# Optimization experiments

Hardware: AMD Instinct MI355X
Metric: run time of the kernel (lower is better)

## Reference

```python
import jax, jax.numpy as jnp
import numpy as np

H = 4        # num_heads
KNN = 10     # k_knn neighbors gathered by distance
KS = 4       # k_select top-k neighbors kept by attention score
EPS = 1e-5
BIG = 1e9


def _ln(x, g, b):
    m = x.mean(-1, keepdims=True)
    v = ((x - m) ** 2).mean(-1, keepdims=True)
    return (x - m) * jax.lax.rsqrt(v + EPS) * g + b


def _sparse_dyn_voxel_attn(x, coords, mask, w_qkv, b_qkv, w_proj, b_proj):
    # x: [B,N,C], coords: [B,N,3], mask: [B,N] bool
    B, N, C = x.shape
    dh = C // H
    qkv = x @ w_qkv + b_qkv                       # [B,N,3C]
    q, k, v = jnp.split(qkv, 3, axis=-1)
    q = q.reshape(B, N, H, dh).transpose(0, 2, 1, 3)   # [B,H,N,dh]
    k = k.reshape(B, N, H, dh).transpose(0, 2, 1, 3)
    v = v.reshape(B, N, H, dh).transpose(0, 2, 1, 3)

    # KNN over voxel coordinates; empty voxels pushed to far distance
    d2 = jnp.sum((coords[:, :, None, :] - coords[:, None, :, :]) ** 2, axis=-1)  # [B,N,N]
    d2 = jnp.where(mask[:, None, :], d2, BIG)
    _, nbr = jax.lax.top_k(-d2, KNN)              # [B,N,KNN] nearest-neighbor indices

    # gather neighbor keys/values: [B,H,N,KNN,dh]
    kn = jax.vmap(lambda a, i: a[:, i, :])(k, nbr)
    vn = jax.vmap(lambda a, i: a[:, i, :])(v, nbr)
    nmask = jax.vmap(lambda m, i: m[i])(mask, nbr)  # [B,N,KNN]

    scale = float(1.0 / np.sqrt(dh))
    scores = jnp.einsum('bhnd,bhnkd->bhnk', q, kn) * scale  # [B,H,N,KNN]
    scores = scores + jnp.where(nmask, 0.0, -BIG)[:, None, :, :]

    # dynamic selection: keep top k_select neighbors by score, softmax over them
    sv, si = jax.lax.top_k(scores, KS)            # [B,H,N,KS]
    w = jax.nn.softmax(sv, axis=-1)
    vsel = jnp.take_along_axis(vn, si[..., None], axis=3)   # [B,H,N,KS,dh]
    o = jnp.einsum('bhnk,bhnkd->bhnd', w, vsel)   # [B,H,N,dh]
    o = o.transpose(0, 2, 1, 3).reshape(B, N, C) @ w_proj + b_proj
    return jnp.where(mask[..., None], o, 0.0)


def setup_inputs() -> dict:
    key = jax.random.key(0)
    ks = jax.random.split(key, 8)
    B, N, C, M = 4, 4096, 64, 256  # N = 16^3 voxels
    s = lambda k, sh: jax.random.normal(k, sh, jnp.float32) * 0.02
    return dict(
        inputs=jax.random.normal(ks[0], (B, N, C), jnp.float32),
        voxel_coords=jax.random.uniform(ks[1], (B, N, 3), jnp.float32) * 16.0,
        non_empty_mask=jax.random.randint(ks[2], (B, N), 0, 2).astype(bool),
        ln1_g=jnp.ones(C, jnp.float32), ln1_b=jnp.zeros(C, jnp.float32),
        ln2_g=jnp.ones(C, jnp.float32), ln2_b=jnp.zeros(C, jnp.float32),
        w_qkv=s(ks[3], (C, 3 * C)), b_qkv=jnp.zeros(3 * C, jnp.float32),
        w_proj=s(ks[4], (C, C)), b_proj=jnp.zeros(C, jnp.float32),
        w1=s(ks[5], (C, M)), b1=jnp.zeros(M, jnp.float32),
        w2=s(ks[6], (M, C)), b2=jnp.zeros(C, jnp.float32),
    )


def reference(inputs, voxel_coords, non_empty_mask, ln1_g, ln1_b, ln2_g, ln2_b,
              w_qkv, b_qkv, w_proj, b_proj, w1, b1, w2, b2):
    a = _sparse_dyn_voxel_attn(_ln(inputs, ln1_g, ln1_b), voxel_coords,
                               non_empty_mask, w_qkv, b_qkv, w_proj, b_proj)
    x = 0.5 * a + inputs                          # drop_path(attn)*0.5 + shortcut (eval)
    h = jax.nn.gelu(_ln(x, ln2_g, ln2_b) @ w1 + b1) @ w2 + b2
    return 0.5 * h + x
```

## Files before the change

kernel.cpp:

```cpp
#include <hip/hip_runtime.h>
#include <hip/hip_bf16.h>
#include <math.h>

#define NH   4
#define DH   16
#define CH   64
#define KNN  10
#define KS   4
#define NV   4096
#define NB   4
#define MHID 256
#define BN   (NB * NV)

#define P_LN1G  0
#define P_LN1B  64
#define P_LN2G  128
#define P_LN2B  192
#define P_WQKV  256
#define P_BQKV  12544
#define P_WPROJ 12736
#define P_BPROJ 16832
#define P_W1    16896
#define P_B1    33280
#define P_W2    33536
#define P_B2    49920
#define P_TOT   49984

#define N_ING  (BN * CH + NB * NV * 3 + P_TOT + BN)
#define N_ING4 (N_ING / 4)
#define N_PACK (16384 + 16384 + 12288)

typedef __hip_bfloat16 bf16;
typedef __attribute__((ext_vector_type(8))) short short8;
typedef __attribute__((ext_vector_type(4))) float float4a;

__device__ __forceinline__ float b2f(bf16 x) { return __bfloat162float(x); }

__device__ __forceinline__ float cvt(const void* p, int i, int isbf) {
  return isbf ? b2f(((const bf16*)p)[i]) : ((const float*)p)[i];
}

__device__ __forceinline__ float us2f(unsigned short u) {
  return __uint_as_float(((unsigned)u) << 16);
}

__device__ __forceinline__ float4 cvt4(const void* p, int i, int isbf) {
  float4 r;
  if (isbf) {
    ushort4 u = *(const ushort4*)((const unsigned short*)p + i);
    r.x = us2f(u.x); r.y = us2f(u.y); r.z = us2f(u.z); r.w = us2f(u.w);
  } else {
    r = *(const float4*)((const float*)p + i);
  }
  return r;
}

__device__ __forceinline__ float wave_sum_f32(float v) {
#pragma unroll
  for (int m = 32; m >= 1; m >>= 1) v += __shfl_xor(v, m, 64);
  return v;
}

__device__ __forceinline__ int wave_sum_i32(int v) {
#pragma unroll
  for (int m = 32; m >= 1; m >>= 1) v += __shfl_xor(v, m, 64);
  return v;
}

__device__ __forceinline__ void wave_min_kv(unsigned& hi, unsigned& lo) {
#pragma unroll
  for (int m = 32; m >= 1; m >>= 1) {
    unsigned ohi = __shfl_xor(hi, m, 64);
    unsigned olo = __shfl_xor(lo, m, 64);
    if (ohi < hi || (ohi == hi && olo < lo)) { hi = ohi; lo = olo; }
  }
}

__device__ __forceinline__ float tanh_fast(float u) {
  float e = __expf(2.0f * u);
  return 1.0f - 2.0f / (e + 1.0f);
}

__device__ __forceinline__ float d2f(float x, float y, float z,
                                     float qx, float qy, float qz) {
  float dx = x - qx, dy = y - qy, dz = z - qz;
  return dx * dx + dy * dy + dz * dz;
}

__device__ __forceinline__ void knn_insert(unsigned long long* arr,
                                           unsigned long long key) {
  if (key < arr[KNN - 1]) {
#pragma unroll
    for (int t = 0; t < KNN; ++t) {
      unsigned long long a = arr[t];
      bool lt = key < a;
      unsigned long long mn = lt ? key : a;
      unsigned long long mx = lt ? a : key;
      arr[t] = mn;
      key = mx;
    }
  }
}

__global__ __launch_bounds__(256) void k_prep(
    const void* xin, const void* coords, const void* maskr,
    const void* ln1g, const void* ln1b, const void* ln2g, const void* ln2b,
    const void* wqkv, const void* bqkv, const void* wproj, const void* bproj,
    const void* w1, const void* b1, const void* w2, const void* b2,
    float* __restrict__ xcan, float* __restrict__ ccan,
    float* __restrict__ pcan, int* __restrict__ mcan,
    unsigned short* __restrict__ w1p, unsigned short* __restrict__ w2p,
    unsigned short* __restrict__ wqp, int* __restrict__ flags)
{
  __shared__ int sfl[2];
  const int tid = threadIdx.x;
  if (tid < 64) {
    const unsigned short* xu = (const unsigned short*)xin;
    const unsigned* mu = (const unsigned*)maskr;
    int cnt = 0;
#pragma unroll
    for (int k = 0; k < 4; ++k) {
      unsigned short w = xu[tid * 4 + k];
      int e = (w >> 7) & 0xFF;
      cnt += (e >= 100 && e <= 140);
    }
#pragma unroll
    for (int m = 32; m >= 1; m >>= 1) cnt += __shfl_xor(cnt, m, 64);
    unsigned big = (mu[tid] > 1u) ? 1u : 0u;
#pragma unroll
    for (int m = 32; m >= 1; m >>= 1) big |= __shfl_xor(big, m, 64);
    if (tid == 0) {
      sfl[0] = (cnt >= 205) ? 1 : 0;
      sfl[1] = big ? 1 : 0;
      if (blockIdx.x == 0) { flags[0] = sfl[0]; flags[1] = sfl[1]; }
    }
  }
  __syncthreads();
  const int isbf = sfl[0], m8 = sfl[1];

  int id = blockIdx.x * 256 + tid;
  if (id < N_ING4) {
    int e4 = id * 4;
    const int n0 = BN * CH, n1 = NB * NV * 3, n2 = P_TOT;
    if (e4 < n0) { *(float4*)&xcan[e4] = cvt4(xin, e4, isbf); return; }
    e4 -= n0;
    if (e4 < n1) { *(float4*)&ccan[e4] = cvt4(coords, e4, isbf); return; }
    e4 -= n1;
    if (e4 < n2) {
      const void* src; int off;
      if      (e4 < P_LN1B)  { src = ln1g;  off = e4 - P_LN1G; }
      else if (e4 < P_LN2G)  { src = ln1b;  off = e4 - P_LN1B; }
      else if (e4 < P_LN2B)  { src = ln2g;  off = e4 - P_LN2G; }
      else if (e4 < P_WQKV)  { src = ln2b;  off = e4 - P_LN2B; }
      else if (e4 < P_BQKV)  { src = wqkv;  off = e4 - P_WQKV; }
      else if (e4 < P_WPROJ) { src = bqkv;  off = e4 - P_BQKV; }
      else if (e4 < P_BPROJ) { src = wproj; off = e4 - P_WPROJ; }
      else if (e4 < P_W1)    { src = bproj; off = e4 - P_BPROJ; }
      else if (e4 < P_B1)    { src = w1;    off = e4 - P_W1; }
      else if (e4 < P_W2)    { src = b1;    off = e4 - P_B1; }
      else if (e4 < P_B2)    { src = w2;    off = e4 - P_W2; }
      else                   { src = b2;    off = e4 - P_B2; }
      *(float4*)&pcan[e4] = cvt4(src, off, isbf);
      return;
    }
    e4 -= n2;
    if (m8) {
      uchar4 u = *(const uchar4*)((const unsigned char*)maskr + e4);
      mcan[e4 + 0] = u.x != 0; mcan[e4 + 1] = u.y != 0;
      mcan[e4 + 2] = u.z != 0; mcan[e4 + 3] = u.w != 0;
    } else {
      int4 v = *(const int4*)((const int*)maskr + e4);
      mcan[e4 + 0] = v.x != 0; mcan[e4 + 1] = v.y != 0;
      mcan[e4 + 2] = v.z != 0; mcan[e4 + 3] = v.w != 0;
    }
    return;
  }
  id -= N_ING4;
  if (id < 16384) {
    int j = id & 7, l = (id >> 3) & 63, kh = (id >> 9) & 1, nt = id >> 10;
    int k = kh * 32 + ((l >> 4) * 8) + j;
    int n = nt * 16 + (l & 15);
    w1p[id] = __bfloat16_as_ushort(__float2bfloat16(cvt(w1, k * MHID + n, isbf)));
    return;
  }
  id -= 16384;
  if (id < 16384) {
    int j = id & 7, l = (id >> 3) & 63, kh = (id >> 9) & 7, nt = id >> 12;
    int k = kh * 32 + ((l >> 4) * 8) + j;
    int n = nt * 16 + (l & 15);
    w2p[id] = __bfloat16_as_ushort(__float2bfloat16(cvt(w2, k * CH + n, isbf)));
    return;
  }
  id -= 16384;
  if (id < 12288) {
    int j = id & 7, l = (id >> 3) & 63, kh = (id >> 9) & 1, nt = id >> 10;
    int k = kh * 32 + ((l >> 4) * 8) + j;
    int n = nt * 16 + (l & 15);
    wqp[id] = __bfloat16_as_ushort(__float2bfloat16(cvt(wqkv, k * 192 + n, isbf)));
  }
}

#define XQS 72
__global__ __launch_bounds__(256) void k_ln_qkv(
    const float* __restrict__ x, const float* __restrict__ pcan,
    const unsigned short* __restrict__ wqp, float* __restrict__ qkv)
{
  __shared__ unsigned short xnb[16 * XQS];
  const int tid = threadIdx.x;
  const int wave = tid >> 6, lane = tid & 63;
  const int row0 = blockIdx.x * 16;

  {
    const float gg = pcan[P_LN1G + lane], bb = pcan[P_LN1B + lane];
#pragma unroll
    for (int r = 0; r < 4; ++r) {
      int m = wave * 4 + r;
      float v = x[(size_t)(row0 + m) * CH + lane];
      float mn = wave_sum_f32(v) * (1.0f / 64.0f);
      float d = v - mn;
      float var = wave_sum_f32(d * d) * (1.0f / 64.0f);
      float rs = 1.0f / sqrtf(var + 1e-5f);
      xnb[m * XQS + lane] =
          __bfloat16_as_ushort(__float2bfloat16(d * rs * gg + bb));
    }
  }
  __syncthreads();

  const int q = lane >> 4, c = lane & 15;
  short8 a0 = *(const short8*)&xnb[c * XQS + q * 8];
  short8 a1 = *(const short8*)&xnb[c * XQS + 32 + q * 8];

#pragma unroll
  for (int t = 0; t < 3; ++t) {
    int nt = wave * 3 + t;
    short8 b0 = *(const short8*)&wqp[(size_t)((nt * 2 + 0) * 64 + lane) * 8];
    short8 b1 = *(const short8*)&wqp[(size_t)((nt * 2 + 1) * 64 + lane) * 8];
    float4a z = {0.f, 0.f, 0.f, 0.f};
    z = __builtin_amdgcn_mfma_f32_16x16x32_bf16(a0, b0, z, 0, 0, 0);
    z = __builtin_amdgcn_mfma_f32_16x16x32_bf16(a1, b1, z, 0, 0, 0);
    int n = nt * 16 + c;
    float bq = pcan[P_BQKV + n];
#pragma unroll
    for (int r = 0; r < 4; ++r) {
      int m = q * 4 + r;
      qkv[(size_t)(row0 + m) * 192 + n] = z[r] + bq;
    }
  }
}

__global__ __launch_bounds__(1024) void k_bin(
    const float* __restrict__ ccan, const int* __restrict__ mcan,
    float4* __restrict__ pbin, unsigned* __restrict__ bstart)
{
  __shared__ unsigned cnt[NV];
  __shared__ unsigned woff[16];
  const int b = blockIdx.x, tid = threadIdx.x;
  const float* cb = ccan + (size_t)b * NV * 3;
  const int* mb = mcan + b * NV;
  unsigned* st = bstart + (size_t)b * 4104;

#pragma unroll
  for (int k = 0; k < 4; ++k) cnt[tid + k * 1024] = 0;
  __syncthreads();

#pragma unroll
  for (int k = 0; k < 4; ++k) {
    int j = tid + k * 1024;
    if (mb[j]) {
      int cx = (int)cb[j * 3];     cx = cx > 15 ? 15 : cx;
      int cy = (int)cb[j * 3 + 1]; cy = cy > 15 ? 15 : cy;
      int cz = (int)cb[j * 3 + 2]; cz = cz > 15 ? 15 : cz;
      atomicAdd(&cnt[(cz << 8) + (cy << 4) + cx], 1u);
    }
  }
  __syncthreads();

  unsigned s0 = cnt[tid * 4], s1 = cnt[tid * 4 + 1];
  unsigned s2 = cnt[tid * 4 + 2], s3 = cnt[tid * 4 + 3];
  unsigned tot = s0 + s1 + s2 + s3;
  unsigned v = tot;
  const int wv = tid >> 6, ln = tid & 63;
#pragma unroll
  for (int d = 1; d < 64; d <<= 1) {
    unsigned o = __shfl_up(v, d, 64);
    if (ln >= d) v += o;
  }
  if (ln == 63) woff[wv] = v;
  __syncthreads();
  unsigned wpre = 0;
  for (int w = 0; w < wv; ++w) wpre += woff[w];
  unsigned r = wpre + v - tot;
  cnt[tid * 4]     = r; st[tid * 4]     = r; r += s0;
  cnt[tid * 4 + 1] = r; st[tid * 4 + 1] = r; r += s1;
  cnt[tid * 4 + 2] = r; st[tid * 4 + 2] = r; r += s2;
  cnt[tid * 4 + 3] = r; st[tid * 4 + 3] = r; r += s3;
  if (tid == 1023) st[4096] = r;
  __syncthreads();

#pragma unroll
  for (int k = 0; k < 4; ++k) {
    int j = tid + k * 1024;
    if (mb[j]) {
      float x = cb[j * 3], y = cb[j * 3 + 1], z = cb[j * 3 + 2];
      int cx = (int)x; cx = cx > 15 ? 15 : cx;
      int cy = (int)y; cy = cy > 15 ? 15 : cy;
      int cz = (int)z; cz = cz > 15 ? 15 : cz;
      unsigned pos = atomicAdd(&cnt[(cz << 8) + (cy << 4) + cx], 1u);
      float4 q; q.x = x; q.y = y; q.z = z; q.w = __int_as_float(j);
      pbin[(size_t)b * NV + pos] = q;
    }
  }
}

__global__ __launch_bounds__(256) void k_knn4(
    const float4* __restrict__ pbin, const unsigned* __restrict__ bstart,
    int* __restrict__ nbr)
{
  const int wave = threadIdx.x >> 6, lane = threadIdx.x & 63;
  const int b = blockIdx.x >> 10;
  const int slot = (blockIdx.x & 1023) * 4 + wave;
  const unsigned* st = bstart + (size_t)b * 4104;
  const int nval = (int)st[4096];
  if (slot >= nval) return;
  const float4* gpt = pbin + (size_t)b * NV;

  const float4 me = gpt[slot];
  const float qx = me.x, qy = me.y, qz = me.z;
  const int qi = __float_as_int(me.w);
  int cz = (int)qz; cz = cz > 15 ? 15 : cz;

  unsigned long long arr[KNN];
#pragma unroll
  for (int t = 0; t < KNN; ++t) arr[t] = ~0ull;

  int R = 2;
  int zlo = cz - 2 < 0 ? 0 : cz - 2;
  int zhi = cz + 2 > 15 ? 15 : cz + 2;
  {
    const int s = (int)st[zlo << 8], e = (int)st[(zhi + 1) << 8];
    for (int i = s + lane; i < e; i += 64) {
      float4 p = gpt[i];
      float d2 = d2f(p.x, p.y, p.z, qx, qy, qz);
      knn_insert(arr, ((unsigned long long)__float_as_uint(d2) << 32) |
                      (unsigned)__float_as_int(p.w));
    }
  }

  for (;;) {
    const float RR = (float)(R * R);
    int c = 0;
#pragma unroll
    for (int t = 0; t < KNN; ++t) {
      float d = __uint_as_float((unsigned)(arr[t] >> 32));
      c += (d <= RR) ? 1 : 0;
    }
    c = wave_sum_i32(c);
    if (c >= KNN) break;
    if (zlo == 0 && zhi == 15) break;
    ++R;
    const int nzlo = cz - R < 0 ? 0 : cz - R;
    const int nzhi = cz + R > 15 ? 15 : cz + R;
    {
      const int s = (int)st[nzlo << 8], e = (int)st[zlo << 8];
      for (int i = s + lane; i < e; i += 64) {
        float4 p = gpt[i];
        float d2 = d2f(p.x, p.y, p.z, qx, qy, qz);
        knn_insert(arr, ((unsigned long long)__float_as_uint(d2) << 32) |
                        (unsigned)__float_as_int(p.w));
      }
    }
    {
      const int s = (int)st[(zhi + 1) << 8], e = (int)st[(nzhi + 1) << 8];
      for (int i = s + lane; i < e; i += 64) {
        float4 p = gpt[i];
        float d2 = d2f(p.x, p.y, p.z, qx, qy, qz);
        knn_insert(arr, ((unsigned long long)__float_as_uint(d2) << 32) |
                        (unsigned)__float_as_int(p.w));
      }
    }
    zlo = nzlo; zhi = nzhi;
  }

  unsigned myj = 0;
#pragma unroll 1
  for (int r = 0; r < KNN; ++r) {
    unsigned hi = (unsigned)(arr[0] >> 32);
    unsigned lo = (unsigned)(arr[0] & 0xffffffffu);
    wave_min_kv(hi, lo);
    const unsigned long long win = ((unsigned long long)hi << 32) | lo;
    if (arr[0] == win) {
#pragma unroll
      for (int t = 0; t < KNN - 1; ++t) arr[t] = arr[t + 1];
      arr[KNN - 1] = ~0ull;
    }
    if (lane == r) myj = lo;
  }
  const int row = (b << 12) | qi;
  if (lane < KNN) nbr[(size_t)row * KNN + lane] = (int)(myj & (NV - 1));
}

#define XNS 72
#define GS  264
__global__ __launch_bounds__(256) void k_attn_mlp(
    const float* __restrict__ qkv, const int* __restrict__ nbr,
    const int* __restrict__ mcan, const float* __restrict__ xcan,
    const float* __restrict__ pcan,
    const unsigned short* __restrict__ w1p,
    const unsigned short* __restrict__ w2p,
    const int* __restrict__ flags, void* __restrict__ out)
{
  __shared__ float wp[CH * CH];
  __shared__ float bp[CH];
  __shared__ float otile[16][CH];
  __shared__ float xtile[16][CH];
  __shared__ float sc[4][NH][KNN];
  __shared__ float wsel[4][NH][KS];
  __shared__ int   isel[4][NH][KS];
  __shared__ int   nb[4][KNN];
  __shared__ float npen[4][KNN];
  __shared__ unsigned short xnb[16 * XNS];
  __shared__ unsigned short gb[16 * GS];
  const int tid = threadIdx.x;
  const int wave = tid >> 6, lane = tid & 63;
  const int row0 = blockIdx.x * 16;
  const int b = row0 / NV;

  {
    const float4* src = (const float4*)(pcan + P_WPROJ);
    float4* dst = (float4*)wp;
    for (int i = tid; i < CH * CH / 4; i += 256) dst[i] = src[i];
    if (tid < CH) bp[tid] = pcan[P_BPROJ + tid];
  }
  __syncthreads();

#pragma unroll 1
  for (int r = 0; r < 4; ++r) {
    const int m = wave * 4 + r;
    const int row = row0 + m;
    if (mcan[row]) {
      if (lane < KNN) {
        int j = nbr[(size_t)row * KNN + lane] & (NV - 1);
        nb[wave][lane] = j;
        npen[wave][lane] = mcan[b * NV + j] ? 0.0f : -1e9f;
      }
      __builtin_amdgcn_wave_barrier();
      if (lane < NH * KNN) {
        int h = lane / KNN, kk = lane % KNN;
        int j = nb[wave][kk];
        const float* qp = qkv + (size_t)row * 192 + h * DH;
        const float* kp = qkv + ((size_t)(b * NV + j)) * 192 + 64 + h * DH;
        float acc = 0.f;
#pragma unroll
        for (int d = 0; d < DH; ++d) acc += qp[d] * kp[d];
        sc[wave][h][kk] = acc * 0.25f + npen[wave][kk];
      }
      __builtin_amdgcn_wave_barrier();
      if (lane < NH) {
        int h = lane;
        float sv[KS]; int sj[KS];
        unsigned used = 0;
#pragma unroll
        for (int rr = 0; rr < KS; ++rr) {
          float best = -INFINITY; int bi = 0;
#pragma unroll
          for (int kk = 0; kk < KNN; ++kk) {
            float s = sc[wave][h][kk];
            if (!(used & (1u << kk)) && s > best) { best = s; bi = kk; }
          }
          used |= 1u << bi; sv[rr] = best; sj[rr] = bi;
        }
        float mx = sv[0];
        float e[KS], sum = 0.f;
#pragma unroll
        for (int rr = 0; rr < KS; ++rr) { e[rr] = expf(sv[rr] - mx); sum += e[rr]; }
        float inv = 1.0f / sum;
#pragma unroll
        for (int rr = 0; rr < KS; ++rr) {
          wsel[wave][h][rr] = e[rr] * inv;
          isel[wave][h][rr] = nb[wave][sj[rr]];
        }
      }
      __builtin_amdgcn_wave_barrier();
      {
        int h = lane >> 4, d = lane & 15;
        float o = 0.f;
#pragma unroll
        for (int rr = 0; rr < KS; ++rr) {
          int j = isel[wave][h][rr];
          o += wsel[wave][h][rr] *
               qkv[((size_t)(b * NV + j)) * 192 + 128 + h * DH + d];
        }
        otile[m][lane] = o;
      }
      __builtin_amdgcn_wave_barrier();
    }
  }

#pragma unroll 1
  for (int r = 0; r < 4; ++r) {
    const int m = wave * 4 + r;
    const int row = row0 + m;
    float x = xcan[(size_t)row * CH + lane];
    if (mcan[row]) {
      float acc = bp[lane];
#pragma unroll 4
      for (int cc = 0; cc < CH; ++cc)
        acc = fmaf(otile[m][cc], wp[cc * CH + lane], acc);
      x += 0.5f * acc;
    }
    xtile[m][lane] = x;
  }

  {
    const float gg = pcan[P_LN2G + lane], bb2 = pcan[P_LN2B + lane];
#pragma unroll
    for (int r = 0; r < 4; ++r) {
      int m = wave * 4 + r;
      float v = xtile[m][lane];
      float mn = wave_sum_f32(v) * (1.0f / 64.0f);
      float d = v - mn;
      float var = wave_sum_f32(d * d) * (1.0f / 64.0f);
      float rs = 1.0f / sqrtf(var + 1e-5f);
      xnb[m * XNS + lane] =
          __bfloat16_as_ushort(__float2bfloat16(d * rs * gg + bb2));
    }
  }
  __syncthreads();

  const int q = lane >> 4, c = lane & 15;
  short8 a0 = *(const short8*)&xnb[c * XNS + q * 8];
  short8 a1 = *(const short8*)&xnb[c * XNS + 32 + q * 8];

  float4a acc1[4];
#pragma unroll
  for (int t = 0; t < 4; ++t) {
    int nt = wave * 4 + t;
    short8 b0 = *(const short8*)&w1p[(size_t)((nt * 2 + 0) * 64 + lane) * 8];
    short8 b1 = *(const short8*)&w1p[(size_t)((nt * 2 + 1) * 64 + lane) * 8];
    float4a z = {0.f, 0.f, 0.f, 0.f};
    z = __builtin_amdgcn_mfma_f32_16x16x32_bf16(a0, b0, z, 0, 0, 0);
    z = __builtin_amdgcn_mfma_f32_16x16x32_bf16(a1, b1, z, 0, 0, 0);
    acc1[t] = z;
  }
#pragma unroll
  for (int t = 0; t < 4; ++t) {
    int n = (wave * 4 + t) * 16 + c;
    float bo = pcan[P_B1 + n];
#pragma unroll
    for (int r = 0; r < 4; ++r) {
      float h = acc1[t][r] + bo;
      float u = 0.7978845608028654f * (h + 0.044715f * h * h * h);
      float gv = 0.5f * h * (1.0f + tanh_fast(u));
      gb[(q * 4 + r) * GS + n] = __bfloat16_as_ushort(__float2bfloat16(gv));
    }
  }
  __syncthreads();

  float4a o = {0.f, 0.f, 0.f, 0.f};
#pragma unroll
  for (int kh = 0; kh < 8; ++kh) {
    short8 ag = *(const short8*)&gb[c * GS + kh * 32 + q * 8];
    short8 bg = *(const short8*)&w2p[(size_t)((wave * 8 + kh) * 64 + lane) * 8];
    o = __builtin_amdgcn_mfma_f32_16x16x32_bf16(ag, bg, o, 0, 0, 0);
  }
  {
    int n = wave * 16 + c;
    float b2v = pcan[P_B2 + n];
    const int isbf = flags[0];
#pragma unroll
    for (int r = 0; r < 4; ++r) {
      int m = q * 4 + r;
      size_t idx = (size_t)(row0 + m) * CH + n;
      float val = 0.5f * (o[r] + b2v) + xtile[m][n];
      if (isbf) ((bf16*)out)[idx] = __float2bfloat16(val);
      else      ((float*)out)[idx] = val;
    }
  }
}

extern "C" void kernel_launch(void* const* d_in, const int* in_sizes, int n_in,
                              void* d_out, int out_size, void* d_ws, size_t ws_size,
                              hipStream_t stream)
{
  char* ws = (char*)d_ws;
  float* qkv   = (float*)(ws);
  float* xcan  = (float*)(ws + 16777216);
  float* ccan  = (float*)(ws + 20971520);
  float* pcan  = (float*)(ws + 21168128);
  int*   mcan  = (int*)  (ws + 21368064);
  int*   nbr   = (int*)  (ws + 21433600);
  int*   flags = (int*)  (ws + 22088960);
  unsigned short* w1p = (unsigned short*)(ws + 22089728);
  unsigned short* w2p = (unsigned short*)(ws + 22122496);
  unsigned short* wqp = (unsigned short*)(ws + 22155264);
  float4*   pbin   = (float4*)  (ws + 22179840);
  unsigned* bstart = (unsigned*)(ws + 22441984);

  const int total = N_ING4 + N_PACK;
  k_prep<<<(total + 255) / 256, 256, 0, stream>>>(
      d_in[0], d_in[1], d_in[2], d_in[3], d_in[4], d_in[5], d_in[6],
      d_in[7], d_in[8], d_in[9], d_in[10], d_in[11], d_in[12], d_in[13], d_in[14],
      xcan, ccan, pcan, mcan, w1p, w2p, wqp, flags);
  k_bin<<<NB, 1024, 0, stream>>>(ccan, mcan, pbin, bstart);
  k_ln_qkv<<<BN / 16, 256, 0, stream>>>(xcan, pcan, wqp, qkv);
  k_knn4<<<NB * (NV / 4), 256, 0, stream>>>(pbin, bstart, nbr);
  k_attn_mlp<<<BN / 16, 256, 0, stream>>>(qkv, nbr, mcan, xcan, pcan,
                                          w1p, w2p, flags, d_out);
}
```

Before: 150.7 us.

## Merge binning into prep kernel and fuse KNN with LN+QKV launch

```diff
diff --git a/kernel.cpp b/kernel.cpp
--- a/kernel.cpp
+++ b/kernel.cpp
@@ -26,9 +26,11 @@
 #define P_B2    49920
 #define P_TOT   49984
 
-#define N_ING  (BN * CH + NB * NV * 3 + P_TOT + BN)
+#define N_ING  (BN * CH + P_TOT + BN)
 #define N_ING4 (N_ING / 4)
 #define N_PACK (16384 + 16384 + 12288)
+#define NPREP  ((N_ING4 + N_PACK + 255) / 256)
+#define KNNBLK (NB * (NV / 4))
 
 typedef __hip_bfloat16 bf16;
 typedef __attribute__((ext_vector_type(8))) short short8;
@@ -107,45 +109,107 @@
     const void* ln1g, const void* ln1b, const void* ln2g, const void* ln2b,
     const void* wqkv, const void* bqkv, const void* wproj, const void* bproj,
     const void* w1, const void* b1, const void* w2, const void* b2,
-    float* __restrict__ xcan, float* __restrict__ ccan,
+    float* __restrict__ xcan,
     float* __restrict__ pcan, int* __restrict__ mcan,
     unsigned short* __restrict__ w1p, unsigned short* __restrict__ w2p,
-    unsigned short* __restrict__ wqp, int* __restrict__ flags)
+    unsigned short* __restrict__ wqp, int* __restrict__ flags,
+    float4* __restrict__ pbin, unsigned* __restrict__ bstart)
 {
   __shared__ int sfl[2];
+  __shared__ unsigned cnt[NV];
+  __shared__ unsigned woff[4];
   const int tid = threadIdx.x;
   if (tid < 64) {
     const unsigned short* xu = (const unsigned short*)xin;
     const unsigned* mu = (const unsigned*)maskr;
-    int cnt = 0;
+    int c = 0;
 #pragma unroll
     for (int k = 0; k < 4; ++k) {
       unsigned short w = xu[tid * 4 + k];
       int e = (w >> 7) & 0xFF;
-      cnt += (e >= 100 && e <= 140);
-    }
-#pragma unroll
-    for (int m = 32; m >= 1; m >>= 1) cnt += __shfl_xor(cnt, m, 64);
+      c += (e >= 100 && e <= 140);
+    }
+#pragma unroll
+    for (int m = 32; m >= 1; m >>= 1) c += __shfl_xor(c, m, 64);
     unsigned big = (mu[tid] > 1u) ? 1u : 0u;
 #pragma unroll
     for (int m = 32; m >= 1; m >>= 1) big |= __shfl_xor(big, m, 64);
     if (tid == 0) {
-      sfl[0] = (cnt >= 205) ? 1 : 0;
+      sfl[0] = (c >= 205) ? 1 : 0;
       sfl[1] = big ? 1 : 0;
       if (blockIdx.x == 0) { flags[0] = sfl[0]; flags[1] = sfl[1]; }
     }
   }
   __syncthreads();
   const int isbf = sfl[0], m8 = sfl[1];
+
+  if (blockIdx.x >= NPREP) {
+    const int bb = blockIdx.x - NPREP;
+    unsigned* st = bstart + (size_t)bb * 4104;
+    const unsigned char* m8p = (const unsigned char*)maskr + (size_t)bb * NV;
+    const int* m32p = (const int*)maskr + (size_t)bb * NV;
+#pragma unroll
+    for (int k = 0; k < 16; ++k) cnt[tid + k * 256] = 0;
+    __syncthreads();
+    for (int k = 0; k < 16; ++k) {
+      int j = tid + k * 256;
+      int mv = m8 ? (m8p[j] != 0) : (m32p[j] != 0);
+      if (mv) {
+        int e = (bb * NV + j) * 3;
+        float x = cvt(coords, e, isbf), y = cvt(coords, e + 1, isbf),
+              z = cvt(coords, e + 2, isbf);
+        int cx = (int)x; cx = cx > 15 ? 15 : cx;
+        int cy = (int)y; cy = cy > 15 ? 15 : cy;
+        int cz = (int)z; cz = cz > 15 ? 15 : cz;
+        atomicAdd(&cnt[(cz << 8) + (cy << 4) + cx], 1u);
+      }
+    }
+    __syncthreads();
+    unsigned s[16], tot = 0;
+#pragma unroll
+    for (int t = 0; t < 16; ++t) { s[t] = cnt[tid * 16 + t]; tot += s[t]; }
+    unsigned v = tot;
+    const int ln = tid & 63, wv = tid >> 6;
+#pragma unroll
+    for (int d = 1; d < 64; d <<= 1) {
+      unsigned o = __shfl_up(v, d, 64);
+      if (ln >= d) v += o;
+    }
+    if (ln == 63) woff[wv] = v;
+    __syncthreads();
+    unsigned wpre = 0;
+    for (int w = 0; w < wv; ++w) wpre += woff[w];
+    unsigned r = wpre + v - tot;
+#pragma unroll
+    for (int t = 0; t < 16; ++t) {
+      cnt[tid * 16 + t] = r; st[tid * 16 + t] = r; r += s[t];
+    }
+    if (tid == 255) st[4096] = r;
+    __syncthreads();
+    for (int k = 0; k < 16; ++k) {
+      int j = tid + k * 256;
+      int mv = m8 ? (m8p[j] != 0) : (m32p[j] != 0);
+      if (mv) {
+        int e = (bb * NV + j) * 3;
+        float x = cvt(coords, e, isbf), y = cvt(coords, e + 1, isbf),
+              z = cvt(coords, e + 2, isbf);
+        int cx = (int)x; cx = cx > 15 ? 15 : cx;
+        int cy = (int)y; cy = cy > 15 ? 15 : cy;
+        int cz = (int)z; cz = cz > 15 ? 15 : cz;
+        unsigned pos = atomicAdd(&cnt[(cz << 8) + (cy << 4) + cx], 1u);
+        float4 q; q.x = x; q.y = y; q.z = z; q.w = __int_as_float(j);
+        pbin[(size_t)bb * NV + pos] = q;
+      }
+    }
+    return;
+  }
 
   int id = blockIdx.x * 256 + tid;
   if (id < N_ING4) {
     int e4 = id * 4;
-    const int n0 = BN * CH, n1 = NB * NV * 3, n2 = P_TOT;
+    const int n0 = BN * CH, n2 = P_TOT;
     if (e4 < n0) { *(float4*)&xcan[e4] = cvt4(xin, e4, isbf); return; }
     e4 -= n0;
-    if (e4 < n1) { *(float4*)&ccan[e4] = cvt4(coords, e4, isbf); return; }
-    e4 -= n1;
     if (e4 < n2) {
       const void* src; int off;
       if      (e4 < P_LN1B)  { src = ln1g;  off = e4 - P_LN1G; }
@@ -169,9 +233,9 @@
       mcan[e4 + 0] = u.x != 0; mcan[e4 + 1] = u.y != 0;
       mcan[e4 + 2] = u.z != 0; mcan[e4 + 3] = u.w != 0;
     } else {
-      int4 v = *(const int4*)((const int*)maskr + e4);
-      mcan[e4 + 0] = v.x != 0; mcan[e4 + 1] = v.y != 0;
-      mcan[e4 + 2] = v.z != 0; mcan[e4 + 3] = v.w != 0;
+      int4 vv = *(const int4*)((const int*)maskr + e4);
+      mcan[e4 + 0] = vv.x != 0; mcan[e4 + 1] = vv.y != 0;
+      mcan[e4 + 2] = vv.z != 0; mcan[e4 + 3] = vv.w != 0;
     }
     return;
   }
@@ -201,15 +265,100 @@
 }
 
 #define XQS 72
-__global__ __launch_bounds__(256) void k_ln_qkv(
+__global__ __launch_bounds__(256) void k_mid(
+    const float4* __restrict__ pbin, const unsigned* __restrict__ bstart,
+    int* __restrict__ nbr,
     const float* __restrict__ x, const float* __restrict__ pcan,
     const unsigned short* __restrict__ wqp, float* __restrict__ qkv)
 {
   __shared__ unsigned short xnb[16 * XQS];
-  const int tid = threadIdx.x;
-  const int wave = tid >> 6, lane = tid & 63;
-  const int row0 = blockIdx.x * 16;
-
+  const int wave = threadIdx.x >> 6, lane = threadIdx.x & 63;
+
+  if (blockIdx.x < KNNBLK) {
+    const int b = blockIdx.x >> 10;
+    const int slot = (blockIdx.x & 1023) * 4 + wave;
+    const unsigned* st = bstart + (size_t)b * 4104;
+    const int nval = (int)st[4096];
+    if (slot >= nval) return;
+    const float4* gpt = pbin + (size_t)b * NV;
+
+    const float4 me = gpt[slot];
+    const float qx = me.x, qy = me.y, qz = me.z;
+    const int qi = __float_as_int(me.w);
+    int cz = (int)qz; cz = cz > 15 ? 15 : cz;
+
+    unsigned long long arr[KNN];
+#pragma unroll
+    for (int t = 0; t < KNN; ++t) arr[t] = ~0ull;
+
+    int R = 2;
+    int zlo = cz - 2 < 0 ? 0 : cz - 2;
+    int zhi = cz + 2 > 15 ? 15 : cz + 2;
+    {
+      const int s = (int)st[zlo << 8], e = (int)st[(zhi + 1) << 8];
+      for (int i = s + lane; i < e; i += 64) {
+        float4 p = gpt[i];
+        float d2 = d2f(p.x, p.y, p.z, qx, qy, qz);
+        knn_insert(arr, ((unsigned long long)__float_as_uint(d2) << 32) |
+                        (unsigned)__float_as_int(p.w));
+      }
+    }
+
+    for (;;) {
+      const float RR = (float)(R * R);
+      int c = 0;
+#pragma unroll
+      for (int t = 0; t < KNN; ++t) {
+        float d = __uint_as_float((unsigned)(arr[t] >> 32));
+        c += (d <= RR) ? 1 : 0;
+      }
+      c = wave_sum_i32(c);
+      if (c >= KNN) break;
+      if (zlo == 0 && zhi == 15) break;
+      ++R;
+      const int nzlo = cz - R < 0 ? 0 : cz - R;
+      const int nzhi = cz + R > 15 ? 15 : cz + R;
+      {
+        const int s = (int)st[nzlo << 8], e = (int)st[zlo << 8];
+        for (int i = s + lane; i < e; i += 64) {
+          float4 p = gpt[i];
+          float d2 = d2f(p.x, p.y, p.z, qx, qy, qz);
+          knn_insert(arr, ((unsigned long long)__float_as_uint(d2) << 32) |
+                          (unsigned)__float_as_int(p.w));
+        }
+      }
+      {
+        const int s = (int)st[(zhi + 1) << 8], e = (int)st[(nzhi + 1) << 8];
+        for (int i = s + lane; i < e; i += 64) {
+          float4 p = gpt[i];
+          float d2 = d2f(p.x, p.y, p.z, qx, qy, qz);
+          knn_insert(arr, ((unsigned long long)__float_as_uint(d2) << 32) |
+                          (unsigned)__float_as_int(p.w));
+        }
+      }
+      zlo = nzlo; zhi = nzhi;
+    }
+
+    unsigned myj = 0;
+#pragma unroll 1
+    for (int r = 0; r < KNN; ++r) {
+      unsigned hi = (unsigned)(arr[0] >> 32);
+      unsigned lo = (unsigned)(arr[0] & 0xffffffffu);
+      wave_min_kv(hi, lo);
+      const unsigned long long win = ((unsigned long long)hi << 32) | lo;
+      if (arr[0] == win) {
+#pragma unroll
+        for (int t = 0; t < KNN - 1; ++t) arr[t] = arr[t + 1];
+        arr[KNN - 1] = ~0ull;
+      }
+      if (lane == r) myj = lo;
+    }
+    const int row = (b << 12) | qi;
+    if (lane < KNN) nbr[(size_t)row * KNN + lane] = (int)(myj & (NV - 1));
+    return;
+  }
+
+  const int row0 = (blockIdx.x - KNNBLK) * 16;
   {
     const float gg = pcan[P_LN1G + lane], bb = pcan[P_LN1B + lane];
 #pragma unroll
@@ -246,157 +395,6 @@
       qkv[(size_t)(row0 + m) * 192 + n] = z[r] + bq;
     }
   }
-}
-
-__global__ __launch_bounds__(1024) void k_bin(
-    const float* __restrict__ ccan, const int* __restrict__ mcan,
-    float4* __restrict__ pbin, unsigned* __restrict__ bstart)
-{
-  __shared__ unsigned cnt[NV];
-  __shared__ unsigned woff[16];
-  const int b = blockIdx.x, tid = threadIdx.x;
-  const float* cb = ccan + (size_t)b * NV * 3;
-  const int* mb = mcan + b * NV;
-  unsigned* st = bstart + (size_t)b * 4104;
-
-#pragma unroll
-  for (int k = 0; k < 4; ++k) cnt[tid + k * 1024] = 0;
-  __syncthreads();
-
-#pragma unroll
-  for (int k = 0; k < 4; ++k) {
-    int j = tid + k * 1024;
-    if (mb[j]) {
-      int cx = (int)cb[j * 3];     cx = cx > 15 ? 15 : cx;
-      int cy = (int)cb[j * 3 + 1]; cy = cy > 15 ? 15 : cy;
-      int cz = (int)cb[j * 3 + 2]; cz = cz > 15 ? 15 : cz;
-      atomicAdd(&cnt[(cz << 8) + (cy << 4) + cx], 1u);
-    }
-  }
-  __syncthreads();
-
-  unsigned s0 = cnt[tid * 4], s1 = cnt[tid * 4 + 1];
-  unsigned s2 = cnt[tid * 4 + 2], s3 = cnt[tid * 4 + 3];
-  unsigned tot = s0 + s1 + s2 + s3;
-  unsigned v = tot;
-  const int wv = tid >> 6, ln = tid & 63;
-#pragma unroll
-  for (int d = 1; d < 64; d <<= 1) {
-    unsigned o = __shfl_up(v, d, 64);
-    if (ln >= d) v += o;
-  }
-  if (ln == 63) woff[wv] = v;
-  __syncthreads();
-  unsigned wpre = 0;
-  for (int w = 0; w < wv; ++w) wpre += woff[w];
-  unsigned r = wpre + v - tot;
-  cnt[tid * 4]     = r; st[tid * 4]     = r; r += s0;
-  cnt[tid * 4 + 1] = r; st[tid * 4 + 1] = r; r += s1;
-  cnt[tid * 4 + 2] = r; st[tid * 4 + 2] = r; r += s2;
-  cnt[tid * 4 + 3] = r; st[tid * 4 + 3] = r; r += s3;
-  if (tid == 1023) st[4096] = r;
-  __syncthreads();
-
-#pragma unroll
-  for (int k = 0; k < 4; ++k) {
-    int j = tid + k * 1024;
-    if (mb[j]) {
-      float x = cb[j * 3], y = cb[j * 3 + 1], z = cb[j * 3 + 2];
-      int cx = (int)x; cx = cx > 15 ? 15 : cx;
-      int cy = (int)y; cy = cy > 15 ? 15 : cy;
-      int cz = (int)z; cz = cz > 15 ? 15 : cz;
-      unsigned pos = atomicAdd(&cnt[(cz << 8) + (cy << 4) + cx], 1u);
-      float4 q; q.x = x; q.y = y; q.z = z; q.w = __int_as_float(j);
-      pbin[(size_t)b * NV + pos] = q;
-    }
-  }
-}
-
-__global__ __launch_bounds__(256) void k_knn4(
-    const float4* __restrict__ pbin, const unsigned* __restrict__ bstart,
-    int* __restrict__ nbr)
-{
-  const int wave = threadIdx.x >> 6, lane = threadIdx.x & 63;
-  const int b = blockIdx.x >> 10;
-  const int slot = (blockIdx.x & 1023) * 4 + wave;
-  const unsigned* st = bstart + (size_t)b * 4104;
-  const int nval = (int)st[4096];
-  if (slot >= nval) return;
-  const float4* gpt = pbin + (size_t)b * NV;
-
-  const float4 me = gpt[slot];
-  const float qx = me.x, qy = me.y, qz = me.z;
-  const int qi = __float_as_int(me.w);
-  int cz = (int)qz; cz = cz > 15 ? 15 : cz;
-
-  unsigned long long arr[KNN];
-#pragma unroll
-  for (int t = 0; t < KNN; ++t) arr[t] = ~0ull;
-
-  int R = 2;
-  int zlo = cz - 2 < 0 ? 0 : cz - 2;
-  int zhi = cz + 2 > 15 ? 15 : cz + 2;
-  {
-    const int s = (int)st[zlo << 8], e = (int)st[(zhi + 1) << 8];
-    for (int i = s + lane; i < e; i += 64) {
-      float4 p = gpt[i];
-      float d2 = d2f(p.x, p.y, p.z, qx, qy, qz);
-      knn_insert(arr, ((unsigned long long)__float_as_uint(d2) << 32) |
-                      (unsigned)__float_as_int(p.w));
-    }
-  }
-
-  for (;;) {
-    const float RR = (float)(R * R);
-    int c = 0;
-#pragma unroll
-    for (int t = 0; t < KNN; ++t) {
-      float d = __uint_as_float((unsigned)(arr[t] >> 32));
-      c += (d <= RR) ? 1 : 0;
-    }
-    c = wave_sum_i32(c);
-    if (c >= KNN) break;
-    if (zlo == 0 && zhi == 15) break;
-    ++R;
-    const int nzlo = cz - R < 0 ? 0 : cz - R;
-    const int nzhi = cz + R > 15 ? 15 : cz + R;
-    {
-      const int s = (int)st[nzlo << 8], e = (int)st[zlo << 8];
-      for (int i = s + lane; i < e; i += 64) {
-        float4 p = gpt[i];
-        float d2 = d2f(p.x, p.y, p.z, qx, qy, qz);
-        knn_insert(arr, ((unsigned long long)__float_as_uint(d2) << 32) |
-                        (unsigned)__float_as_int(p.w));
-      }
-    }
-    {
-      const int s = (int)st[(zhi + 1) << 8], e = (int)st[(nzhi + 1) << 8];
-      for (int i = s + lane; i < e; i += 64) {
-        float4 p = gpt[i];
-        float d2 = d2f(p.x, p.y, p.z, qx, qy, qz);
-        knn_insert(arr, ((unsigned long long)__float_as_uint(d2) << 32) |
-                        (unsigned)__float_as_int(p.w));
-      }
-    }
-    zlo = nzlo; zhi = nzhi;
-  }
-
-  unsigned myj = 0;
-#pragma unroll 1
-  for (int r = 0; r < KNN; ++r) {
-    unsigned hi = (unsigned)(arr[0] >> 32);
-    unsigned lo = (unsigned)(arr[0] & 0xffffffffu);
-    wave_min_kv(hi, lo);
-    const unsigned long long win = ((unsigned long long)hi << 32) | lo;
-    if (arr[0] == win) {
-#pragma unroll
-      for (int t = 0; t < KNN - 1; ++t) arr[t] = arr[t + 1];
-      arr[KNN - 1] = ~0ull;
-    }
-    if (lane == r) myj = lo;
-  }
-  const int row = (b << 12) | qi;
-  if (lane < KNN) nbr[(size_t)row * KNN + lane] = (int)(myj & (NV - 1));
 }
 
 #define XNS 72
@@ -585,7 +583,6 @@
   char* ws = (char*)d_ws;
   float* qkv   = (float*)(ws);
   float* xcan  = (float*)(ws + 16777216);
-  float* ccan  = (float*)(ws + 20971520);
   float* pcan  = (float*)(ws + 21168128);
   int*   mcan  = (int*)  (ws + 21368064);
   int*   nbr   = (int*)  (ws + 21433600);
@@ -596,14 +593,12 @@
   float4*   pbin   = (float4*)  (ws + 22179840);
   unsigned* bstart = (unsigned*)(ws + 22441984);
 
-  const int total = N_ING4 + N_PACK;
-  k_prep<<<(total + 255) / 256, 256, 0, stream>>>(
+  k_prep<<<NPREP + NB, 256, 0, stream>>>(
       d_in[0], d_in[1], d_in[2], d_in[3], d_in[4], d_in[5], d_in[6],
       d_in[7], d_in[8], d_in[9], d_in[10], d_in[11], d_in[12], d_in[13], d_in[14],
-      xcan, ccan, pcan, mcan, w1p, w2p, wqp, flags);
-  k_bin<<<NB, 1024, 0, stream>>>(ccan, mcan, pbin, bstart);
-  k_ln_qkv<<<BN / 16, 256, 0, stream>>>(xcan, pcan, wqp, qkv);
-  k_knn4<<<NB * (NV / 4), 256, 0, stream>>>(pbin, bstart, nbr);
+      xcan, pcan, mcan, w1p, w2p, wqp, flags, pbin, bstart);
+  k_mid<<<KNNBLK + BN / 16, 256, 0, stream>>>(pbin, bstart, nbr,
+                                              xcan, pcan, wqp, qkv);
   k_attn_mlp<<<BN / 16, 256, 0, stream>>>(qkv, nbr, mcan, xcan, pcan,
                                           w1p, w2p, flags, d_out);
 }
```

New measurement: 158.1 us. 1.05x slower.

## Bin points into z-y columns and search a 2D window in KNN

Applied to the files above, without the earlier changes.

```diff
diff --git a/kernel.cpp b/kernel.cpp
--- a/kernel.cpp
+++ b/kernel.cpp
@@ -33,6 +33,7 @@
 typedef __hip_bfloat16 bf16;
 typedef __attribute__((ext_vector_type(8))) short short8;
 typedef __attribute__((ext_vector_type(4))) float float4a;
+typedef unsigned long long ull;
 
 __device__ __forceinline__ float b2f(bf16 x) { return __bfloat162float(x); }
 
@@ -61,12 +62,6 @@
   return v;
 }
 
-__device__ __forceinline__ int wave_sum_i32(int v) {
-#pragma unroll
-  for (int m = 32; m >= 1; m >>= 1) v += __shfl_xor(v, m, 64);
-  return v;
-}
-
 __device__ __forceinline__ void wave_min_kv(unsigned& hi, unsigned& lo) {
 #pragma unroll
   for (int m = 32; m >= 1; m >>= 1) {
@@ -87,15 +82,14 @@
   return dx * dx + dy * dy + dz * dz;
 }
 
-__device__ __forceinline__ void knn_insert(unsigned long long* arr,
-                                           unsigned long long key) {
+__device__ __forceinline__ void knn_insert(ull* arr, ull key) {
   if (key < arr[KNN - 1]) {
 #pragma unroll
     for (int t = 0; t < KNN; ++t) {
-      unsigned long long a = arr[t];
+      ull a = arr[t];
       bool lt = key < a;
-      unsigned long long mn = lt ? key : a;
-      unsigned long long mx = lt ? a : key;
+      ull mn = lt ? key : a;
+      ull mx = lt ? a : key;
       arr[t] = mn;
       key = mx;
     }
@@ -117,20 +111,20 @@
   if (tid < 64) {
     const unsigned short* xu = (const unsigned short*)xin;
     const unsigned* mu = (const unsigned*)maskr;
-    int cnt = 0;
+    int c = 0;
 #pragma unroll
     for (int k = 0; k < 4; ++k) {
       unsigned short w = xu[tid * 4 + k];
       int e = (w >> 7) & 0xFF;
-      cnt += (e >= 100 && e <= 140);
-    }
-#pragma unroll
-    for (int m = 32; m >= 1; m >>= 1) cnt += __shfl_xor(cnt, m, 64);
+      c += (e >= 100 && e <= 140);
+    }
+#pragma unroll
+    for (int m = 32; m >= 1; m >>= 1) c += __shfl_xor(c, m, 64);
     unsigned big = (mu[tid] > 1u) ? 1u : 0u;
 #pragma unroll
     for (int m = 32; m >= 1; m >>= 1) big |= __shfl_xor(big, m, 64);
     if (tid == 0) {
-      sfl[0] = (cnt >= 205) ? 1 : 0;
+      sfl[0] = (c >= 205) ? 1 : 0;
       sfl[1] = big ? 1 : 0;
       if (blockIdx.x == 0) { flags[0] = sfl[0]; flags[1] = sfl[1]; }
     }
@@ -169,9 +163,9 @@
       mcan[e4 + 0] = u.x != 0; mcan[e4 + 1] = u.y != 0;
       mcan[e4 + 2] = u.z != 0; mcan[e4 + 3] = u.w != 0;
     } else {
-      int4 v = *(const int4*)((const int*)maskr + e4);
-      mcan[e4 + 0] = v.x != 0; mcan[e4 + 1] = v.y != 0;
-      mcan[e4 + 2] = v.z != 0; mcan[e4 + 3] = v.w != 0;
+      int4 vv = *(const int4*)((const int*)maskr + e4);
+      mcan[e4 + 0] = vv.x != 0; mcan[e4 + 1] = vv.y != 0;
+      mcan[e4 + 2] = vv.z != 0; mcan[e4 + 3] = vv.w != 0;
     }
     return;
   }
@@ -197,6 +191,63 @@
     int k = kh * 32 + ((l >> 4) * 8) + j;
     int n = nt * 16 + (l & 15);
     wqp[id] = __bfloat16_as_ushort(__float2bfloat16(cvt(wqkv, k * 192 + n, isbf)));
+  }
+}
+
+__global__ __launch_bounds__(1024) void k_bin(
+    const float* __restrict__ ccan, const int* __restrict__ mcan,
+    float4* __restrict__ pbin, unsigned* __restrict__ lstart)
+{
+  __shared__ unsigned cnt[256];
+  const int b = blockIdx.x, tid = threadIdx.x;
+  const float* cb = ccan + (size_t)b * NV * 3;
+  const int* mb = mcan + b * NV;
+  unsigned* st = lstart + b * 260;
+
+  if (tid < 256) cnt[tid] = 0;
+  __syncthreads();
+
+#pragma unroll
+  for (int k = 0; k < 4; ++k) {
+    int j = tid + k * 1024;
+    if (mb[j]) {
+      int cy = (int)cb[j * 3 + 1]; cy = cy > 15 ? 15 : cy;
+      int cz = (int)cb[j * 3 + 2]; cz = cz > 15 ? 15 : cz;
+      atomicAdd(&cnt[(cz << 4) + cy], 1u);
+    }
+  }
+  __syncthreads();
+
+  if (tid < 64) {
+    unsigned s0 = cnt[tid * 4], s1 = cnt[tid * 4 + 1];
+    unsigned s2 = cnt[tid * 4 + 2], s3 = cnt[tid * 4 + 3];
+    unsigned tot = s0 + s1 + s2 + s3;
+    unsigned v = tot;
+#pragma unroll
+    for (int d = 1; d < 64; d <<= 1) {
+      unsigned o = __shfl_up(v, d, 64);
+      if (tid >= d) v += o;
+    }
+    unsigned r = v - tot;
+    cnt[tid * 4]     = r; st[tid * 4]     = r; r += s0;
+    cnt[tid * 4 + 1] = r; st[tid * 4 + 1] = r; r += s1;
+    cnt[tid * 4 + 2] = r; st[tid * 4 + 2] = r; r += s2;
+    cnt[tid * 4 + 3] = r; st[tid * 4 + 3] = r; r += s3;
+    if (tid == 63) st[256] = v;
+  }
+  __syncthreads();
+
+#pragma unroll
+  for (int k = 0; k < 4; ++k) {
+    int j = tid + k * 1024;
+    if (mb[j]) {
+      float x = cb[j * 3], y = cb[j * 3 + 1], z = cb[j * 3 + 2];
+      int cy = (int)y; cy = cy > 15 ? 15 : cy;
+      int cz = (int)z; cz = cz > 15 ? 15 : cz;
+      unsigned pos = atomicAdd(&cnt[(cz << 4) + cy], 1u);
+      float4 q; q.x = x; q.y = y; q.z = z; q.w = __int_as_float(j);
+      pbin[(size_t)b * NV + pos] = q;
+    }
   }
 }
 
@@ -248,105 +299,42 @@
   }
 }
 
-__global__ __launch_bounds__(1024) void k_bin(
-    const float* __restrict__ ccan, const int* __restrict__ mcan,
-    float4* __restrict__ pbin, unsigned* __restrict__ bstart)
-{
-  __shared__ unsigned cnt[NV];
-  __shared__ unsigned woff[16];
-  const int b = blockIdx.x, tid = threadIdx.x;
-  const float* cb = ccan + (size_t)b * NV * 3;
-  const int* mb = mcan + b * NV;
-  unsigned* st = bstart + (size_t)b * 4104;
-
-#pragma unroll
-  for (int k = 0; k < 4; ++k) cnt[tid + k * 1024] = 0;
-  __syncthreads();
-
-#pragma unroll
-  for (int k = 0; k < 4; ++k) {
-    int j = tid + k * 1024;
-    if (mb[j]) {
-      int cx = (int)cb[j * 3];     cx = cx > 15 ? 15 : cx;
-      int cy = (int)cb[j * 3 + 1]; cy = cy > 15 ? 15 : cy;
-      int cz = (int)cb[j * 3 + 2]; cz = cz > 15 ? 15 : cz;
-      atomicAdd(&cnt[(cz << 8) + (cy << 4) + cx], 1u);
-    }
-  }
-  __syncthreads();
-
-  unsigned s0 = cnt[tid * 4], s1 = cnt[tid * 4 + 1];
-  unsigned s2 = cnt[tid * 4 + 2], s3 = cnt[tid * 4 + 3];
-  unsigned tot = s0 + s1 + s2 + s3;
-  unsigned v = tot;
-  const int wv = tid >> 6, ln = tid & 63;
-#pragma unroll
-  for (int d = 1; d < 64; d <<= 1) {
-    unsigned o = __shfl_up(v, d, 64);
-    if (ln >= d) v += o;
-  }
-  if (ln == 63) woff[wv] = v;
-  __syncthreads();
-  unsigned wpre = 0;
-  for (int w = 0; w < wv; ++w) wpre += woff[w];
-  unsigned r = wpre + v - tot;
-  cnt[tid * 4]     = r; st[tid * 4]     = r; r += s0;
-  cnt[tid * 4 + 1] = r; st[tid * 4 + 1] = r; r += s1;
-  cnt[tid * 4 + 2] = r; st[tid * 4 + 2] = r; r += s2;
-  cnt[tid * 4 + 3] = r; st[tid * 4 + 3] = r; r += s3;
-  if (tid == 1023) st[4096] = r;
-  __syncthreads();
-
-#pragma unroll
-  for (int k = 0; k < 4; ++k) {
-    int j = tid + k * 1024;
-    if (mb[j]) {
-      float x = cb[j * 3], y = cb[j * 3 + 1], z = cb[j * 3 + 2];
-      int cx = (int)x; cx = cx > 15 ? 15 : cx;
-      int cy = (int)y; cy = cy > 15 ? 15 : cy;
-      int cz = (int)z; cz = cz > 15 ? 15 : cz;
-      unsigned pos = atomicAdd(&cnt[(cz << 8) + (cy << 4) + cx], 1u);
-      float4 q; q.x = x; q.y = y; q.z = z; q.w = __int_as_float(j);
-      pbin[(size_t)b * NV + pos] = q;
-    }
-  }
-}
-
-__global__ __launch_bounds__(256) void k_knn4(
-    const float4* __restrict__ pbin, const unsigned* __restrict__ bstart,
+__global__ __launch_bounds__(256) void k_knn6(
+    const float4* __restrict__ pbin, const unsigned* __restrict__ lstart,
     int* __restrict__ nbr)
 {
   const int wave = threadIdx.x >> 6, lane = threadIdx.x & 63;
   const int b = blockIdx.x >> 10;
   const int slot = (blockIdx.x & 1023) * 4 + wave;
-  const unsigned* st = bstart + (size_t)b * 4104;
-  const int nval = (int)st[4096];
+  const unsigned* st = lstart + b * 260;
+  const int nval = (int)st[256];
   if (slot >= nval) return;
   const float4* gpt = pbin + (size_t)b * NV;
 
   const float4 me = gpt[slot];
   const float qx = me.x, qy = me.y, qz = me.z;
   const int qi = __float_as_int(me.w);
+  int cy = (int)qy; cy = cy > 15 ? 15 : cy;
   int cz = (int)qz; cz = cz > 15 ? 15 : cz;
 
-  unsigned long long arr[KNN];
-#pragma unroll
-  for (int t = 0; t < KNN; ++t) arr[t] = ~0ull;
-
-  int R = 2;
-  int zlo = cz - 2 < 0 ? 0 : cz - 2;
-  int zhi = cz + 2 > 15 ? 15 : cz + 2;
-  {
-    const int s = (int)st[zlo << 8], e = (int)st[(zhi + 1) << 8];
-    for (int i = s + lane; i < e; i += 64) {
-      float4 p = gpt[i];
-      float d2 = d2f(p.x, p.y, p.z, qx, qy, qz);
-      knn_insert(arr, ((unsigned long long)__float_as_uint(d2) << 32) |
-                      (unsigned)__float_as_int(p.w));
-    }
-  }
-
-  for (;;) {
+  ull arr[KNN];
+  for (int R = 2;; ++R) {
+    const int zlo = cz - R < 0 ? 0 : cz - R, zhi = cz + R > 15 ? 15 : cz + R;
+    const int ylo = cy - R < 0 ? 0 : cy - R, yhi = cy + R > 15 ? 15 : cy + R;
+#pragma unroll
+    for (int t = 0; t < KNN; ++t) arr[t] = ~0ull;
+
+    for (int z = zlo; z <= zhi; ++z) {
+      const int s = (int)st[(z << 4) + ylo];
+      const int e = (int)st[(z << 4) + yhi + 1];
+      for (int i = s + lane; i < e; i += 64) {
+        float4 p = gpt[i];
+        float d2 = d2f(p.x, p.y, p.z, qx, qy, qz);
+        knn_insert(arr, ((ull)__float_as_uint(d2) << 32) |
+                        (unsigned)__float_as_int(p.w));
+      }
+    }
+
     const float RR = (float)(R * R);
     int c = 0;
 #pragma unroll
@@ -354,31 +342,10 @@
       float d = __uint_as_float((unsigned)(arr[t] >> 32));
       c += (d <= RR) ? 1 : 0;
     }
-    c = wave_sum_i32(c);
-    if (c >= KNN) break;
-    if (zlo == 0 && zhi == 15) break;
-    ++R;
-    const int nzlo = cz - R < 0 ? 0 : cz - R;
-    const int nzhi = cz + R > 15 ? 15 : cz + R;
-    {
-      const int s = (int)st[nzlo << 8], e = (int)st[zlo << 8];
-      for (int i = s + lane; i < e; i += 64) {
-        float4 p = gpt[i];
-        float d2 = d2f(p.x, p.y, p.z, qx, qy, qz);
-        knn_insert(arr, ((unsigned long long)__float_as_uint(d2) << 32) |
-                        (unsigned)__float_as_int(p.w));
-      }
-    }
-    {
-      const int s = (int)st[(zhi + 1) << 8], e = (int)st[(nzhi + 1) << 8];
-      for (int i = s + lane; i < e; i += 64) {
-        float4 p = gpt[i];
-        float d2 = d2f(p.x, p.y, p.z, qx, qy, qz);
-        knn_insert(arr, ((unsigned long long)__float_as_uint(d2) << 32) |
-                        (unsigned)__float_as_int(p.w));
-      }
-    }
-    zlo = nzlo; zhi = nzhi;
+    int tot = __popcll(__ballot(c & 1)) + 2 * __popcll(__ballot(c & 2)) +
+              4 * __popcll(__ballot(c & 4)) + 8 * __popcll(__ballot(c & 8));
+    if (tot >= KNN) break;
+    if (zlo == 0 && zhi == 15 && ylo == 0 && yhi == 15) break;
   }
 
   unsigned myj = 0;
@@ -387,7 +354,7 @@
     unsigned hi = (unsigned)(arr[0] >> 32);
     unsigned lo = (unsigned)(arr[0] & 0xffffffffu);
     wave_min_kv(hi, lo);
-    const unsigned long long win = ((unsigned long long)hi << 32) | lo;
+    const ull win = ((ull)hi << 32) | lo;
     if (arr[0] == win) {
 #pragma unroll
       for (int t = 0; t < KNN - 1; ++t) arr[t] = arr[t + 1];
@@ -594,16 +561,16 @@
   unsigned short* w2p = (unsigned short*)(ws + 22122496);
   unsigned short* wqp = (unsigned short*)(ws + 22155264);
   float4*   pbin   = (float4*)  (ws + 22179840);
-  unsigned* bstart = (unsigned*)(ws + 22441984);
+  unsigned* lstart = (unsigned*)(ws + 22441984);
 
   const int total = N_ING4 + N_PACK;
   k_prep<<<(total + 255) / 256, 256, 0, stream>>>(
       d_in[0], d_in[1], d_in[2], d_in[3], d_in[4], d_in[5], d_in[6],
       d_in[7], d_in[8], d_in[9], d_in[10], d_in[11], d_in[12], d_in[13], d_in[14],
       xcan, ccan, pcan, mcan, w1p, w2p, wqp, flags);
-  k_bin<<<NB, 1024, 0, stream>>>(ccan, mcan, pbin, bstart);
+  k_bin<<<NB, 1024, 0, stream>>>(ccan, mcan, pbin, lstart);
   k_ln_qkv<<<BN / 16, 256, 0, stream>>>(xcan, pcan, wqp, qkv);
-  k_knn4<<<NB * (NV / 4), 256, 0, stream>>>(pbin, bstart, nbr);
+  k_knn6<<<NB * (NV / 4), 256, 0, stream>>>(pbin, lstart, nbr);
   k_attn_mlp<<<BN / 16, 256, 0, stream>>>(qkv, nbr, mcan, xcan, pcan,
                                           w1p, w2p, flags, d_out);
 }
```

Result: slower. 154.6 us (+2.6%).
